# Performance work log

Measured on AMD Instinct MI355X. Metric: run time of the kernel, lower is better.

Reference implementation:

```python
import jax, jax.numpy as jnp
import numpy as np

B, N, D = 128, 64, 768
H, DK = 32, 24
L, TE, TD, VP = 4, 32, 40, 512


def setup_inputs():
    key = jax.random.key(0)
    ks = jax.random.split(key, 20)
    s = 0.02
    return {
        "node_reps": jax.random.normal(ks[0], (B, N, D), jnp.float32),
        "distance": jax.random.randint(ks[1], (B, N, N), 0, TD, jnp.int32),
        "connection_reps": jax.random.randint(ks[2], (B, N, N), 0, TE, jnp.int32),
        "shortest_path_feature_trajectory": jax.random.randint(ks[3], (B, N, N, L, 3), 0, VP, jnp.int32),
        "mask": jnp.zeros((B, N), jnp.bool_),
        "W_qkv": jax.random.normal(ks[4], (D, 3 * H * DK), jnp.float32) * s,
        "b_qkv": jnp.zeros((3 * H * DK,), jnp.float32),
        "W_out": jax.random.normal(ks[5], (H * DK, D), jnp.float32) * s,
        "b_out": jnp.zeros((D,), jnp.float32),
        "edge_q_table": jax.random.normal(ks[6], (TE, H, DK), jnp.float32) * s,
        "edge_k_table": jax.random.normal(ks[7], (TE, H, DK), jnp.float32) * s,
        "dist_q_table": jax.random.normal(ks[8], (TD, H, DK), jnp.float32) * s,
        "dist_k_table": jax.random.normal(ks[9], (TD, H, DK), jnp.float32) * s,
        "path_emb": jax.random.normal(ks[10], (VP, H), jnp.float32) * s,
        "path_pos_w": jax.random.normal(ks[11], (L, H), jnp.float32) * s,
        "edge_val_table": jax.random.normal(ks[12], (TE, H, DK), jnp.float32) * s,
        "dist_val_table": jax.random.normal(ks[13], (TD, H, DK), jnp.float32) * s,
        "toeplitz_r": jnp.ones((H, N), jnp.float32) + jax.random.normal(ks[14], (H, N), jnp.float32) * s,
        "toeplitz_c": jnp.ones((H, N), jnp.float32) + jax.random.normal(ks[15], (H, N), jnp.float32) * s,
    }


def _relpos_bias(q, k, types, Eq, Ek):
    # bias[b,h,i,j] = q[b,h,i] . Ek[t(i,j),h] + k[b,h,j] . Eq[t(i,j),h]
    Bx, Hx, Nx, _ = q.shape
    qb = jnp.einsum('bhid,thd->bhit', q, Ek)   # per-type query bias [B,H,N,T]
    kb = jnp.einsum('bhjd,thd->bhtj', k, Eq)   # per-type key bias   [B,H,T,N]
    idx = jnp.broadcast_to(types[:, None], (Bx, Hx, Nx, Nx))
    return jnp.take_along_axis(qb, idx, axis=3) + jnp.take_along_axis(kb, idx, axis=2)


def _path_bias(traj, dist, path_emb, path_pos_w):
    # Graphormer-style shortest-path bias: per-position embedded (3-way) edge
    # features dotted with per-position head weights, normalized by path length.
    bias = 0.0
    for l in range(traj.shape[3]):          # small fixed loop over path positions
        for f in range(3):                  # 3 discrete edge features per hop
            bias = bias + path_emb[traj[:, :, :, l, f]] * path_pos_w[l]  # [B,N,N,H]
    denom = jnp.clip(dist.astype(jnp.float32), 1.0, None)
    return (bias / denom[..., None]).transpose(0, 3, 1, 2)  # [B,H,N,N]


def _comp_values(a, types, Vt):
    # z[b,h,i,d] = sum_j a[b,h,i,j] * Vt[type(i,j),h,d]  (post-softmax value add)
    onehot = jax.nn.one_hot(types, Vt.shape[0], dtype=a.dtype)  # [B,N,N,T]
    s = jnp.einsum('bhij,bijt->bhit', a, onehot)
    return jnp.einsum('bhit,thd->bhid', s, Vt)


def reference(node_reps, distance, connection_reps, shortest_path_feature_trajectory, mask,
              W_qkv, b_qkv, W_out, b_out, edge_q_table, edge_k_table,
              dist_q_table, dist_k_table, path_emb, path_pos_w,
              edge_val_table, dist_val_table, toeplitz_r, toeplitz_c):
    Bx, Nx, Dx = node_reps.shape
    qkv = (node_reps @ W_qkv + b_qkv).reshape(Bx, Nx, 3, H, DK)
    q = qkv[:, :, 0].transpose(0, 2, 1, 3)  # [B,H,N,dk]
    k = qkv[:, :, 1].transpose(0, 2, 1, 3)
    v = qkv[:, :, 2].transpose(0, 2, 1, 3)
    a = jnp.einsum('bhid,bhjd->bhij', q, k)
    a = a + _relpos_bias(q, k, connection_reps, edge_q_table, edge_k_table)
    a = a + _relpos_bias(q, k, distance, dist_q_table, dist_k_table)
    a = a + _path_bias(shortest_path_feature_trajectory, distance, path_emb, path_pos_w)
    a = a * (DK ** -0.5)  # scale applied after bias addition, as in the original
    a = jnp.where(mask[:, None, None, :], -jnp.inf, a)
    a = jax.nn.softmax(a, axis=3)
    # post-softmax per-head Toeplitz modulation: T[h,i,j] = r[h,j-i] (j>=i) else c[h,i-j]
    off = jnp.arange(Nx)[None, :] - jnp.arange(Nx)[:, None]
    toep = jnp.where(off >= 0, toeplitz_r[:, jnp.clip(off, 0)], toeplitz_c[:, jnp.clip(-off, 0)])
    a = a * toep[None]  # attention dropout is identity at eval
    z = jnp.einsum('bhij,bhjd->bhid', a, v)
    z = z + _comp_values(a, connection_reps, edge_val_table)
    z = z + _comp_values(a, distance, dist_val_table)
    z = z.transpose(0, 2, 1, 3).reshape(Bx, Nx, H * DK)
    return z @ W_out + b_out
```

## Files before the change

kernel.cpp:

```cpp
#include <hip/hip_runtime.h>
#include <hip/hip_fp16.h>

#define Bb 128
#define Nn 64
#define Dd 768
#define Hh 32
#define DKk 24
#define Ll 4
#define TEe 32
#define TDd 40

typedef __attribute__((ext_vector_type(8))) short short8_t;
typedef __attribute__((ext_vector_type(8))) _Float16 half8_t;
typedef __attribute__((ext_vector_type(4))) float f32x4;

__device__ __forceinline__ void gload16(const void* g, void* l) {
    __builtin_amdgcn_global_load_lds((const __attribute__((address_space(1))) void*)g,
                                     (__attribute__((address_space(3))) void*)l, 16, 0, 0);
}

__global__ __launch_bounds__(256) void split_f16_kernel(
    const float4* __restrict__ src, __half* __restrict__ hi,
    __half* __restrict__ lo, int n4)
{
    int i = blockIdx.x * 256 + threadIdx.x;
    if (i >= n4) return;
    float4 v = src[i];
    float vv[4] = {v.x, v.y, v.z, v.w};
    unsigned short hbits[4], lbits[4];
#pragma unroll
    for (int e = 0; e < 4; e++) {
        __half h = __float2half(vv[e]);
        __half l = __float2half(vv[e] - __half2float(h));
        hbits[e] = __half_as_ushort(h);
        lbits[e] = __half_as_ushort(l);
    }
    uint2 ph, pl;
    ph.x = (unsigned)hbits[0] | ((unsigned)hbits[1] << 16);
    ph.y = (unsigned)hbits[2] | ((unsigned)hbits[3] << 16);
    pl.x = (unsigned)lbits[0] | ((unsigned)lbits[1] << 16);
    pl.y = (unsigned)lbits[2] | ((unsigned)lbits[3] << 16);
    *(uint2*)&hi[i * 4] = ph;
    *(uint2*)&lo[i * 4] = pl;
}

#define MFMA16(a, b, c) __builtin_amdgcn_mfma_f32_16x16x32_f16((a), (b), (c), 0, 0, 0)

template <typename OutT>
__global__ __launch_bounds__(256, 3) void gemm_f16x2_kernel(
    const __half* __restrict__ Ah, const __half* __restrict__ Al,
    const __half* __restrict__ Bh,
    const float* __restrict__ bias, OutT* __restrict__ C,
    int M, int N, int K)
{
    __shared__ char smem[49152] __attribute__((aligned(16)));

    const int t = threadIdx.x;
    const int lane = t & 63, w = t >> 6;
    const int wr = w >> 1, wc = w & 1;

    const int nbx = gridDim.x;
    int id = blockIdx.y * nbx + blockIdx.x;
    const int nwg = nbx * gridDim.y;
    if ((nwg & 7) == 0) {
        id = (id & 7) * (nwg >> 3) + (id >> 3);
    }
    const int rowBase = (id / nbx) * 128, colBase = (id % nbx) * 128;

    const int m0 = t >> 2;
    const int g0 = (t & 3) ^ ((m0 >> 1) & 3);
    const size_t aoff0 = (size_t)(rowBase + m0) * K + g0 * 8;
    const size_t aoff1 = aoff0 + (size_t)64 * K;
    const size_t boff0 = (size_t)(colBase + m0) * K + g0 * 8;
    const size_t boff1 = boff0 + (size_t)64 * K;
    const int lb = w * 1024;

    int offA[4], offB[4];
    const int lr = lane & 15, koff = lane >> 4;
#pragma unroll
    for (int i = 0; i < 4; i++) {
        int ma = wr * 64 + i * 16 + lr;
        offA[i] = ma * 32 + ((koff ^ ((ma >> 1) & 3)) << 3);
        int nb = wc * 64 + i * 16 + lr;
        offB[i] = nb * 32 + ((koff ^ ((nb >> 1) & 3)) << 3);
    }

    f32x4 acc[4][4];
#pragma unroll
    for (int i = 0; i < 4; i++)
#pragma unroll
        for (int j = 0; j < 4; j++) acc[i][j] = (f32x4){0.f, 0.f, 0.f, 0.f};

    auto stage = [&](int buf, int k0) {
        char* base = smem + buf * 24576;
        gload16(Ah + aoff0 + k0, base + lb);
        gload16(Ah + aoff1 + k0, base + lb + 4096);
        gload16(Al + aoff0 + k0, base + 8192 + lb);
        gload16(Al + aoff1 + k0, base + 8192 + lb + 4096);
        gload16(Bh + boff0 + k0, base + 16384 + lb);
        gload16(Bh + boff1 + k0, base + 16384 + lb + 4096);
    };

    stage(0, 0);
    __syncthreads();

    const int T = K / 32;
    for (int it = 0; it < T; it++) {
        const int cur = it & 1;
        if (it + 1 < T) stage(cur ^ 1, (it + 1) * 32);

        const short* sAh = (const short*)(smem + cur * 24576);
        const short* sAl = (const short*)(smem + cur * 24576 + 8192);
        const short* sBh = (const short*)(smem + cur * 24576 + 16384);

        half8_t ah[4], al[4], bh[4];
#pragma unroll
        for (int i = 0; i < 4; i++) {
            ah[i] = *(const half8_t*)(sAh + offA[i]);
            al[i] = *(const half8_t*)(sAl + offA[i]);
            bh[i] = *(const half8_t*)(sBh + offB[i]);
        }
#pragma unroll
        for (int i = 0; i < 4; i++)
#pragma unroll
            for (int j = 0; j < 4; j++) {
                acc[i][j] = MFMA16(al[i], bh[j], acc[i][j]);
                acc[i][j] = MFMA16(ah[i], bh[j], acc[i][j]);
            }
        __syncthreads();
    }

    const int crow = rowBase + wr * 64 + (lane >> 4) * 4;
    const int ccol = colBase + wc * 64 + (lane & 15);
#pragma unroll
    for (int j = 0; j < 4; j++) {
        int col = ccol + j * 16;
        float bv = bias[col];
#pragma unroll
        for (int i = 0; i < 4; i++) {
#pragma unroll
            for (int r = 0; r < 4; r++) {
                float x = acc[i][j][r] + bv;
                if constexpr (__is_same(OutT, __half))
                    C[(size_t)(crow + i * 16 + r) * N + col] = __float2half(x);
                else
                    C[(size_t)(crow + i * 16 + r) * N + col] = x;
            }
        }
    }
}

__device__ __forceinline__ void do_transpose(
    const float* __restrict__ W, __half* __restrict__ th,
    int K, int N, int k0, int n0, char* uls, int t)
{
    float (*tile)[33] = (float(*)[33])uls;
    const int c = t & 31, r0 = t >> 5;
    for (int rr = r0; rr < 32; rr += 8)
        tile[rr][c] = W[(size_t)(k0 + rr) * N + n0 + c];
    __syncthreads();
    for (int rr = r0; rr < 32; rr += 8)
        th[(size_t)(n0 + rr) * K + k0 + c] = __float2half(tile[c][rr]);
}

__global__ __launch_bounds__(256, 2) void prep_kernel(
    const float* __restrict__ Wqkv, __half* __restrict__ wqth,
    const float* __restrict__ Wout, __half* __restrict__ woth,
    const int* __restrict__ traj, const int* __restrict__ dist,
    const int* __restrict__ conn,
    const float* __restrict__ path_emb, const float* __restrict__ path_pos_w,
    __half* __restrict__ pbias, unsigned short* __restrict__ packed)
{
    __shared__ char uls[69632] __attribute__((aligned(16)));
    const int id = blockIdx.x;
    const int t = threadIdx.x;

    if (id < 1728) {
        do_transpose(Wqkv, wqth, 768, 2304, (id % 24) * 32, (id / 24) * 32, uls, t);
        return;
    }
    if (id < 2304) {
        int id2 = id - 1728;
        do_transpose(Wout, woth, 768, 768, (id2 % 24) * 32, (id2 / 24) * 32, uls, t);
        return;
    }

    __half* sPE  = (__half*)uls;
    __half* sOut = (__half*)(uls + 32768);
    const int q = id - 2304;
    const int b = q >> 3, pt = q & 7;
    const int ch = t & 7;
    const int pl = t >> 3;

    const long pair0 = (long)b * 4096 + pt * 512;

    for (int e = t; e < 512; e += 256) {
        long gp = pair0 + e;
        packed[gp] = (unsigned short)((unsigned)conn[gp] | ((unsigned)dist[gp] << 8));
    }

    for (int e = t; e < 4096; e += 256) {
        float4 v = ((const float4*)path_emb)[e];
        __half2 h0 = __floats2half2_rn(v.x, v.y);
        __half2 h1 = __floats2half2_rn(v.z, v.w);
        uint2 pk;
        pk.x = *(unsigned*)&h0;
        pk.y = *(unsigned*)&h1;
        *(uint2*)&sPE[e * 4] = pk;
    }
    __half2 pwa[4], pwb[4];
#pragma unroll
    for (int l = 0; l < 4; l++) {
        float4 wv = *(const float4*)&path_pos_w[l * 32 + ch * 4];
        pwa[l] = __floats2half2_rn(wv.x, wv.y);
        pwb[l] = __floats2half2_rn(wv.z, wv.w);
    }
    __syncthreads();

    for (int rnd = 0; rnd < 16; rnd++) {
        int p = rnd * 32 + pl;
        long gp = pair0 + p;
        const int4* tp = (const int4*)(traj + gp * 12);
        int4 t0 = tp[0], t1 = tp[1], t2 = tp[2];
        int idxs[12] = {t0.x, t0.y, t0.z, t0.w, t1.x, t1.y, t1.z, t1.w,
                        t2.x, t2.y, t2.z, t2.w};
        __half2 acc0 = __float2half2_rn(0.f);
        __half2 acc1 = __float2half2_rn(0.f);
#pragma unroll
        for (int l = 0; l < 4; l++) {
            uint2 r0 = *(const uint2*)&sPE[idxs[l * 3 + 0] * 32 + ch * 4];
            uint2 r1 = *(const uint2*)&sPE[idxs[l * 3 + 1] * 32 + ch * 4];
            uint2 r2 = *(const uint2*)&sPE[idxs[l * 3 + 2] * 32 + ch * 4];
            __half2 s0 = __hadd2(__hadd2(*(__half2*)&r0.x, *(__half2*)&r1.x), *(__half2*)&r2.x);
            __half2 s1 = __hadd2(__hadd2(*(__half2*)&r0.y, *(__half2*)&r1.y), *(__half2*)&r2.y);
            acc0 = __hfma2(s0, pwa[l], acc0);
            acc1 = __hfma2(s1, pwb[l], acc1);
        }
        int dd = dist[gp];
        __half2 hi2 = __float2half2_rn(1.0f / (float)(dd > 1 ? dd : 1));
        acc0 = __hmul2(acc0, hi2);
        acc1 = __hmul2(acc1, hi2);
        uint2 pk;
        pk.x = *(unsigned*)&acc0;
        pk.y = *(unsigned*)&acc1;
        *(uint2*)&sOut[p * 36 + ch * 4] = pk;
    }
    __syncthreads();

    __half* outBase = pbias + (size_t)b * 32 * 4096 + pt * 512;
    for (int e = t; e < 32 * 512; e += 256) {
        int hh = e >> 9, p = e & 511;
        outBase[(size_t)hh * 4096 + p] = sOut[p * 36 + hh];
    }
}

#define IDX32(row, k) ((row)*32 + (((((k) >> 3) ^ (((row) >> 1) & 3))) << 3) + ((k) & 7))
#define IDX64(row, k) ((row)*64 + (((((k) >> 3) ^ ((row) & 7))) << 3) + ((k) & 7))
#define LDH32(base, row, k) (*(const half8_t*)(sm + (base) + IDX32(row, k) * 2))
#define LDH64(base, row, k) (*(const half8_t*)(sm + (base) + IDX64(row, k) * 2))

__global__ __launch_bounds__(256, 5) void attn_kernel(
    const __half* __restrict__ qkv,
    const unsigned short* __restrict__ packed,
    const __half* __restrict__ pbias,
    const float* __restrict__ eq, const float* __restrict__ ek,
    const float* __restrict__ dq, const float* __restrict__ dk,
    const float* __restrict__ ev, const float* __restrict__ dv,
    const float* __restrict__ tr, const float* __restrict__ tcp,
    __half* __restrict__ zh, __half* __restrict__ zl)
{
    __shared__ char sm[30336] __attribute__((aligned(16)));
    const int h = blockIdx.x, b = blockIdx.y;
    const int t = threadIdx.x;
    const int lane = t & 63, w = t >> 6;
    const int c = lane & 15, kg = lane >> 4;

    enum { TEK = 0, TEQ = 2048, TDK = 4096, TDQ = 7168,
           GQBE = 10240, GKBE = 14592, GQBD = 18944, GKBD = 24384,
           TOEP = 29824,
           PH = 0, VTH = 8192, VET = 12288, VDT = 14336,
           BINE = 17920, BIND = 23040 };

    const size_t qkvRow = (size_t)(b * 64) * 2304 + h * 24;
    const unsigned short* tpk = packed + (size_t)b * 4096;
    const int ibase = 16 * w + kg * 4;

    half8_t zf8 = (half8_t)(_Float16)0.f;
    half8_t aQ = zf8, aK = zf8, bK0 = zf8, bK1 = zf8, bK2 = zf8, bK3 = zf8;
    if (kg < 3) {
        const __half* qp = qkv + qkvRow + kg * 8;
        aQ  = *(const half8_t*)(qp + (size_t)(16 * w + c) * 2304);
        aK  = *(const half8_t*)(qp + (size_t)(16 * w + c) * 2304 + 768);
        bK0 = *(const half8_t*)(qp + (size_t)(c) * 2304 + 768);
        bK1 = *(const half8_t*)(qp + (size_t)(16 + c) * 2304 + 768);
        bK2 = *(const half8_t*)(qp + (size_t)(32 + c) * 2304 + 768);
        bK3 = *(const half8_t*)(qp + (size_t)(48 + c) * 2304 + 768);
    }
    unsigned short tvv[16];
    __half pbvh[16];
    {
        const __half* pbb = pbias + ((size_t)(b * 32 + h)) * 4096;
#pragma unroll
        for (int j4 = 0; j4 < 4; j4++) {
            int jj = 16 * j4 + c;
#pragma unroll
            for (int r = 0; r < 4; r++) {
                int i = ibase + r;
                tvv[j4 * 4 + r] = tpk[i * 64 + jj];
                pbvh[j4 * 4 + r] = pbb[i * 64 + jj];
            }
        }
    }
    short8_t v8 = (short8_t)(short)0;
    const int vi = t / 3, voc = t - vi * 3;
    if (t < 192)
        v8 = *(const short8_t*)(qkv + qkvRow + (size_t)vi * 2304 + 1536 + voc * 8);

    for (int f = t; f < 864; f += 256) {
        int row = f / 6, d0 = (f - row * 6) * 4;
        const float* src; int base, lrow;
        if (row < 32)       { src = ek + ((size_t)row * 32 + h) * 24 + d0; base = TEK; lrow = row; }
        else if (row < 64)  { src = eq + ((size_t)(row - 32) * 32 + h) * 24 + d0; base = TEQ; lrow = row - 32; }
        else if (row < 104) { src = dk + ((size_t)(row - 64) * 32 + h) * 24 + d0; base = TDK; lrow = row - 64; }
        else                { src = dq + ((size_t)(row - 104) * 32 + h) * 24 + d0; base = TDQ; lrow = row - 104; }
        float4 v = *(const float4*)src;
        __half2 p0 = __floats2half2_rn(v.x, v.y);
        __half2 p1 = __floats2half2_rn(v.z, v.w);
        uint2 pk; pk.x = *(unsigned*)&p0; pk.y = *(unsigned*)&p1;
        *(uint2*)(sm + base + IDX32(lrow, d0) * 2) = pk;
    }
    if (t < 208) {
        int base, row, oct;
        if (t < 32)       { base = TEK; row = t; oct = 3; }
        else if (t < 64)  { base = TEQ; row = t - 32; oct = 3; }
        else if (t < 136) { int u = t - 64;
                            if (u < 40) { base = TDK; row = u; oct = 3; }
                            else { int v2 = u - 40; base = TDK; row = 40 + (v2 >> 2); oct = v2 & 3; } }
        else              { int u = t - 136;
                            if (u < 40) { base = TDQ; row = u; oct = 3; }
                            else { int v2 = u - 40; base = TDQ; row = 40 + (v2 >> 2); oct = v2 & 3; } }
        uint4 z4; z4.x = z4.y = z4.z = z4.w = 0u;
        *(uint4*)(sm + base + IDX32(row, oct * 8) * 2) = z4;
    }
    if (t < 64) ((float*)(sm + TOEP))[63 + t] = tr[h * 64 + t];
    else if (t < 127) { int d2 = t - 63; ((float*)(sm + TOEP))[63 - d2] = tcp[h * 64 + d2]; }
    __syncthreads();

    f32x4 accS[4];
    {
        accS[0] = MFMA16(aQ, bK0, ((f32x4){0.f, 0.f, 0.f, 0.f}));
        accS[1] = MFMA16(aQ, bK1, ((f32x4){0.f, 0.f, 0.f, 0.f}));
        accS[2] = MFMA16(aQ, bK2, ((f32x4){0.f, 0.f, 0.f, 0.f}));
        accS[3] = MFMA16(aQ, bK3, ((f32x4){0.f, 0.f, 0.f, 0.f}));
        const int i0 = ibase;
#pragma unroll
        for (int tab = 0; tab < 4; tab++) {
            half8_t aF = (tab == 1 || tab == 3) ? aK : aQ;
            int tabBase = (tab == 0) ? TEK : (tab == 1) ? TEQ : (tab == 2) ? TDK : TDQ;
            int gtBase  = (tab == 0) ? GQBE : (tab == 1) ? GKBE : (tab == 2) ? GQBD : GKBD;
            int ntiles  = (tab < 2) ? 2 : 3;
            int nrows   = (tab < 2) ? 32 : 40;
            for (int t4 = 0; t4 < ntiles; t4++) {
                half8_t bF = LDH32(tabBase, 16 * t4 + c, kg * 8);
                f32x4 a = MFMA16(aF, bF, ((f32x4){0.f, 0.f, 0.f, 0.f}));
                int tcol = 16 * t4 + c;
                if (tcol < nrows) {
                    __half2 p0 = __floats2half2_rn(a[0], a[1]);
                    __half2 p1 = __floats2half2_rn(a[2], a[3]);
                    uint2 pk; pk.x = *(unsigned*)&p0; pk.y = *(unsigned*)&p1;
                    *(uint2*)(sm + gtBase + (tcol * 68 + i0) * 2) = pk;
                }
            }
        }
    }
    __syncthreads();

    {
        float p[4][4];
#pragma unroll
        for (int j4 = 0; j4 < 4; j4++) {
            int jj = 16 * j4 + c;
#pragma unroll
            for (int r = 0; r < 4; r++) {
                int i = ibase + r;
                int ce = (int)(tvv[j4 * 4 + r] & 255u), cd = (int)(tvv[j4 * 4 + r] >> 8);
                float se = __half2float(*(const __half*)(sm + GQBE + (ce * 68 + i) * 2))
                         + __half2float(*(const __half*)(sm + GKBE + (ce * 68 + jj) * 2));
                float sd = __half2float(*(const __half*)(sm + GQBD + (cd * 68 + i) * 2))
                         + __half2float(*(const __half*)(sm + GKBD + (cd * 68 + jj) * 2));
                float s = (accS[j4][r] + __half2float(pbvh[j4 * 4 + r])) + (se + sd);
                p[j4][r] = s * 0.2944888931f;
            }
        }
        float inv[4];
#pragma unroll
        for (int r = 0; r < 4; r++) {
            float m = fmaxf(fmaxf(p[0][r], p[1][r]), fmaxf(p[2][r], p[3][r]));
            m = fmaxf(m, __shfl_xor(m, 1));
            m = fmaxf(m, __shfl_xor(m, 2));
            m = fmaxf(m, __shfl_xor(m, 4));
            m = fmaxf(m, __shfl_xor(m, 8));
            float s = 0.f;
#pragma unroll
            for (int j4 = 0; j4 < 4; j4++) { p[j4][r] = exp2f(p[j4][r] - m); s += p[j4][r]; }
            s += __shfl_xor(s, 1);
            s += __shfl_xor(s, 2);
            s += __shfl_xor(s, 4);
            s += __shfl_xor(s, 8);
            inv[r] = 1.0f / s;
        }
        const float* tp = (const float*)(sm + TOEP);
#pragma unroll
        for (int j4 = 0; j4 < 4; j4++) {
#pragma unroll
            for (int r = 0; r < 4; r++) {
                int i = ibase + r, j = 16 * j4 + c;
                float tpv = tp[63 + j - i];
                float val = p[j4][r] * inv[r] * tpv;
                *(unsigned short*)(sm + PH + IDX64(i, j) * 2) =
                    __half_as_ushort(__float2half(val));
            }
        }
    }
    __syncthreads();

    for (int e = t; e < 2752; e += 256) {
        uint2 z2; z2.x = z2.y = 0u;
        *(uint2*)(sm + 8192 + e * 8) = z2;
    }
    __syncthreads();

    if (t < 192) {
#pragma unroll
        for (int e2 = 0; e2 < 8; e2++) {
            *(short*)(sm + VTH + IDX64(voc * 8 + e2, vi) * 2) = v8[e2];
        }
    }
    for (int f = t; f < 432; f += 256) {
        int tcol = f / 6, d0 = (f - tcol * 6) * 4;
        const float* src = (tcol < 32) ? ev + ((size_t)tcol * 32 + h) * 24 + d0
                                       : dv + ((size_t)(tcol - 32) * 32 + h) * 24 + d0;
        float4 v = *(const float4*)src;
        float vv[4] = {v.x, v.y, v.z, v.w};
#pragma unroll
        for (int r2 = 0; r2 < 4; r2++) {
            int d = d0 + r2;
            if (tcol < 32)
                *(unsigned short*)(sm + VET + IDX32(d, tcol) * 2) =
                    __half_as_ushort(__float2half(vv[r2]));
            else
                *(unsigned short*)(sm + VDT + (d * 56 + (tcol - 32)) * 2) =
                    __half_as_ushort(__float2half(vv[r2]));
        }
    }
    __syncthreads();

    {
        for (int rnd = 0; rnd < 2; rnd++) {
            if ((w >> 1) == rnd) {
                int kind = w & 1;
                int i = lane;
                const unsigned short* ip = tpk + i * 64 + rnd * 32;
                __half* bins = (__half*)(sm + (kind ? BIND : BINE));
                int stride = kind ? 56 : 40;
#pragma unroll
                for (int blk = 0; blk < 4; blk++) {
                    int o = rnd * 4 + blk;
                    short8_t ph8 = *(const short8_t*)(sm + PH + (i * 64 + ((o ^ (i & 7)) << 3)) * 2);
                    uint4 pw = *(const uint4*)(ip + blk * 8);
                    unsigned dw[4] = {pw.x, pw.y, pw.z, pw.w};
#pragma unroll
                    for (int e2 = 0; e2 < 8; e2++) {
                        unsigned ent = (dw[e2 >> 1] >> ((e2 & 1) * 16)) & 0xFFFFu;
                        int ty = kind ? (int)(ent >> 8) : (int)(ent & 255u);
                        __half pv = __ushort_as_half((unsigned short)ph8[e2]);
                        __half* ap = bins + i * stride + ty;
                        *ap = __hadd(*ap, pv);
                    }
                }
            }
            __syncthreads();
        }
    }

    {
        half8_t aP0 = LDH64(PH, 16 * w + c, kg * 8);
        half8_t aP1 = LDH64(PH, 16 * w + c, 32 + kg * 8);
        half8_t aBE = *(const half8_t*)(sm + BINE + ((16 * w + c) * 40 + kg * 8) * 2);
        half8_t aD0 = *(const half8_t*)(sm + BIND + ((16 * w + c) * 56 + kg * 8) * 2);
        half8_t zf = (half8_t)(_Float16)0.f;
        half8_t aD1 = (kg < 2)
            ? *(const half8_t*)(sm + BIND + ((16 * w + c) * 56 + 32 + kg * 8) * 2) : zf;
#pragma unroll
        for (int d4 = 0; d4 < 2; d4++) {
            int drow = 16 * d4 + c;
            f32x4 a = (f32x4){0.f, 0.f, 0.f, 0.f};
            a = MFMA16(aP0, LDH64(VTH, drow, kg * 8), a);
            a = MFMA16(aP1, LDH64(VTH, drow, 32 + kg * 8), a);
            a = MFMA16(aBE, LDH32(VET, drow, kg * 8), a);
            a = MFMA16(aD0, *(const half8_t*)(sm + VDT + (drow * 56 + kg * 8) * 2), a);
            half8_t bD1 = (kg < 2)
                ? *(const half8_t*)(sm + VDT + (drow * 56 + 32 + kg * 8) * 2) : zf;
            a = MFMA16(aD1, bD1, a);
            int d = d4 * 16 + c;
            if (d < 24) {
#pragma unroll
                for (int r = 0; r < 4; r++) {
                    int i = 16 * w + kg * 4 + r;
                    size_t zi = ((size_t)(b * 64 + i)) * 768 + h * 24 + d;
                    float x = a[r];
                    __half hx = __float2half(x);
                    zh[zi] = hx;
                    zl[zi] = __float2half(x - __half2float(hx));
                }
            }
        }
    }
}

extern "C" void kernel_launch(void* const* d_in, const int* in_sizes, int n_in,
                              void* d_out, int out_size, void* d_ws, size_t ws_size,
                              hipStream_t stream) {
    const float* node = (const float*)d_in[0];
    const int* dist   = (const int*)d_in[1];
    const int* conn   = (const int*)d_in[2];
    const int* traj   = (const int*)d_in[3];
    const float* Wqkv = (const float*)d_in[5];
    const float* bqkv = (const float*)d_in[6];
    const float* Wout = (const float*)d_in[7];
    const float* bout = (const float*)d_in[8];
    const float* eqT  = (const float*)d_in[9];
    const float* ekT  = (const float*)d_in[10];
    const float* dqT  = (const float*)d_in[11];
    const float* dkT  = (const float*)d_in[12];
    const float* pemb = (const float*)d_in[13];
    const float* ppw  = (const float*)d_in[14];
    const float* evT  = (const float*)d_in[15];
    const float* dvT  = (const float*)d_in[16];
    const float* trp  = (const float*)d_in[17];
    const float* tcp  = (const float*)d_in[18];
    float* out = (float*)d_out;

    char* ws = (char*)d_ws;
    __half* qkvh = (__half*)ws;
    __half* pb   = (__half*)(ws + 37748736);
    __half* wqth = (__half*)(ws + 71303168);
    __half* woth = (__half*)(ws + 74842112);
    unsigned short* pkd = (unsigned short*)(ws + 76021760);
    __half* nodeh = (__half*)(ws + 109051904);
    __half* nodel = nodeh + 8192 * 768;
    __half* zhp = nodeh;
    __half* zlp = nodel;

    split_f16_kernel<<<6144, 256, 0, stream>>>((const float4*)node, nodeh, nodel,
                                               8192 * 768 / 4);

    prep_kernel<<<3328, 256, 0, stream>>>(Wqkv, wqth, Wout, woth,
                                          traj, dist, conn, pemb, ppw, pb, pkd);

    gemm_f16x2_kernel<__half><<<dim3(18, 64), 256, 0, stream>>>(
        nodeh, nodel, wqth, bqkv, qkvh, 8192, 2304, 768);

    attn_kernel<<<dim3(Hh, Bb), 256, 0, stream>>>(
        qkvh, pkd, pb, eqT, ekT, dqT, dkT, evT, dvT, trp, tcp, zhp, zlp);

    gemm_f16x2_kernel<float><<<dim3(6, 64), 256, 0, stream>>>(
        zhp, zlp, woth, bout, out, 8192, 768, 768);
}
```

Baseline: 327.2 us.

## Fuse node split into prep kernel, shrink its LDS, add MFMA priority hints

```diff
diff --git a/kernel.cpp b/kernel.cpp
--- a/kernel.cpp
+++ b/kernel.cpp
@@ -17,31 +17,6 @@
 __device__ __forceinline__ void gload16(const void* g, void* l) {
     __builtin_amdgcn_global_load_lds((const __attribute__((address_space(1))) void*)g,
                                      (__attribute__((address_space(3))) void*)l, 16, 0, 0);
-}
-
-__global__ __launch_bounds__(256) void split_f16_kernel(
-    const float4* __restrict__ src, __half* __restrict__ hi,
-    __half* __restrict__ lo, int n4)
-{
-    int i = blockIdx.x * 256 + threadIdx.x;
-    if (i >= n4) return;
-    float4 v = src[i];
-    float vv[4] = {v.x, v.y, v.z, v.w};
-    unsigned short hbits[4], lbits[4];
-#pragma unroll
-    for (int e = 0; e < 4; e++) {
-        __half h = __float2half(vv[e]);
-        __half l = __float2half(vv[e] - __half2float(h));
-        hbits[e] = __half_as_ushort(h);
-        lbits[e] = __half_as_ushort(l);
-    }
-    uint2 ph, pl;
-    ph.x = (unsigned)hbits[0] | ((unsigned)hbits[1] << 16);
-    ph.y = (unsigned)hbits[2] | ((unsigned)hbits[3] << 16);
-    pl.x = (unsigned)lbits[0] | ((unsigned)lbits[1] << 16);
-    pl.y = (unsigned)lbits[2] | ((unsigned)lbits[3] << 16);
-    *(uint2*)&hi[i * 4] = ph;
-    *(uint2*)&lo[i * 4] = pl;
 }
 
 #define MFMA16(a, b, c) __builtin_amdgcn_mfma_f32_16x16x32_f16((a), (b), (c), 0, 0, 0)
@@ -163,7 +138,9 @@
         th[(size_t)(n0 + rr) * K + k0 + c] = __float2half(tile[c][rr]);
 }
 
-__global__ __launch_bounds__(256, 2) void prep_kernel(
+__global__ __launch_bounds__(256, 3) void prep_kernel(
+    const float4* __restrict__ node, __half* __restrict__ nodeh,
+    __half* __restrict__ nodel,
     const float* __restrict__ Wqkv, __half* __restrict__ wqth,
     const float* __restrict__ Wout, __half* __restrict__ woth,
     const int* __restrict__ traj, const int* __restrict__ dist,
@@ -171,24 +148,46 @@
     const float* __restrict__ path_emb, const float* __restrict__ path_pos_w,
     __half* __restrict__ pbias, unsigned short* __restrict__ packed)
 {
-    __shared__ char uls[69632] __attribute__((aligned(16)));
+    __shared__ char uls[51200] __attribute__((aligned(16)));
     const int id = blockIdx.x;
     const int t = threadIdx.x;
 
-    if (id < 1728) {
-        do_transpose(Wqkv, wqth, 768, 2304, (id % 24) * 32, (id / 24) * 32, uls, t);
+    if (id >= 3328) {
+        int i = (id - 3328) * 256 + t;
+        if (i >= 8192 * 768 / 4) return;
+        float4 v = node[i];
+        float vv[4] = {v.x, v.y, v.z, v.w};
+        unsigned short hbits[4], lbits[4];
+#pragma unroll
+        for (int e = 0; e < 4; e++) {
+            __half h = __float2half(vv[e]);
+            __half l = __float2half(vv[e] - __half2float(h));
+            hbits[e] = __half_as_ushort(h);
+            lbits[e] = __half_as_ushort(l);
+        }
+        uint2 ph, pl2;
+        ph.x = (unsigned)hbits[0] | ((unsigned)hbits[1] << 16);
+        ph.y = (unsigned)hbits[2] | ((unsigned)hbits[3] << 16);
+        pl2.x = (unsigned)lbits[0] | ((unsigned)lbits[1] << 16);
+        pl2.y = (unsigned)lbits[2] | ((unsigned)lbits[3] << 16);
+        *(uint2*)&nodeh[i * 4] = ph;
+        *(uint2*)&nodel[i * 4] = pl2;
         return;
     }
-    if (id < 2304) {
-        int id2 = id - 1728;
+    if (id >= 2752) {
+        int id2 = id - 2752;
         do_transpose(Wout, woth, 768, 768, (id2 % 24) * 32, (id2 / 24) * 32, uls, t);
         return;
     }
+    if (id >= 1024) {
+        int id2 = id - 1024;
+        do_transpose(Wqkv, wqth, 768, 2304, (id2 % 24) * 32, (id2 / 24) * 32, uls, t);
+        return;
+    }
 
     __half* sPE  = (__half*)uls;
     __half* sOut = (__half*)(uls + 32768);
-    const int q = id - 2304;
-    const int b = q >> 3, pt = q & 7;
+    const int b = id >> 3, pt = id & 7;
     const int ch = t & 7;
     const int pl = t >> 3;
 
@@ -217,40 +216,42 @@
     }
     __syncthreads();
 
-    for (int rnd = 0; rnd < 16; rnd++) {
-        int p = rnd * 32 + pl;
-        long gp = pair0 + p;
-        const int4* tp = (const int4*)(traj + gp * 12);
-        int4 t0 = tp[0], t1 = tp[1], t2 = tp[2];
-        int idxs[12] = {t0.x, t0.y, t0.z, t0.w, t1.x, t1.y, t1.z, t1.w,
-                        t2.x, t2.y, t2.z, t2.w};
-        __half2 acc0 = __float2half2_rn(0.f);
-        __half2 acc1 = __float2half2_rn(0.f);
-#pragma unroll
-        for (int l = 0; l < 4; l++) {
-            uint2 r0 = *(const uint2*)&sPE[idxs[l * 3 + 0] * 32 + ch * 4];
-            uint2 r1 = *(const uint2*)&sPE[idxs[l * 3 + 1] * 32 + ch * 4];
-            uint2 r2 = *(const uint2*)&sPE[idxs[l * 3 + 2] * 32 + ch * 4];
-            __half2 s0 = __hadd2(__hadd2(*(__half2*)&r0.x, *(__half2*)&r1.x), *(__half2*)&r2.x);
-            __half2 s1 = __hadd2(__hadd2(*(__half2*)&r0.y, *(__half2*)&r1.y), *(__half2*)&r2.y);
-            acc0 = __hfma2(s0, pwa[l], acc0);
-            acc1 = __hfma2(s1, pwb[l], acc1);
-        }
-        int dd = dist[gp];
-        __half2 hi2 = __float2half2_rn(1.0f / (float)(dd > 1 ? dd : 1));
-        acc0 = __hmul2(acc0, hi2);
-        acc1 = __hmul2(acc1, hi2);
-        uint2 pk;
-        pk.x = *(unsigned*)&acc0;
-        pk.y = *(unsigned*)&acc1;
-        *(uint2*)&sOut[p * 36 + ch * 4] = pk;
-    }
-    __syncthreads();
-
-    __half* outBase = pbias + (size_t)b * 32 * 4096 + pt * 512;
-    for (int e = t; e < 32 * 512; e += 256) {
-        int hh = e >> 9, p = e & 511;
-        outBase[(size_t)hh * 4096 + p] = sOut[p * 36 + hh];
+    for (int cchunk = 0; cchunk < 2; cchunk++) {
+        for (int rr = 0; rr < 8; rr++) {
+            int p_local = rr * 32 + pl;
+            long gp = pair0 + cchunk * 256 + p_local;
+            const int4* tp = (const int4*)(traj + gp * 12);
+            int4 t0 = tp[0], t1 = tp[1], t2 = tp[2];
+            int idxs[12] = {t0.x, t0.y, t0.z, t0.w, t1.x, t1.y, t1.z, t1.w,
+                            t2.x, t2.y, t2.z, t2.w};
+            __half2 acc0 = __float2half2_rn(0.f);
+            __half2 acc1 = __float2half2_rn(0.f);
+#pragma unroll
+            for (int l = 0; l < 4; l++) {
+                uint2 r0 = *(const uint2*)&sPE[idxs[l * 3 + 0] * 32 + ch * 4];
+                uint2 r1 = *(const uint2*)&sPE[idxs[l * 3 + 1] * 32 + ch * 4];
+                uint2 r2 = *(const uint2*)&sPE[idxs[l * 3 + 2] * 32 + ch * 4];
+                __half2 s0 = __hadd2(__hadd2(*(__half2*)&r0.x, *(__half2*)&r1.x), *(__half2*)&r2.x);
+                __half2 s1 = __hadd2(__hadd2(*(__half2*)&r0.y, *(__half2*)&r1.y), *(__half2*)&r2.y);
+                acc0 = __hfma2(s0, pwa[l], acc0);
+                acc1 = __hfma2(s1, pwb[l], acc1);
+            }
+            int dd = dist[gp];
+            __half2 hi2 = __float2half2_rn(1.0f / (float)(dd > 1 ? dd : 1));
+            acc0 = __hmul2(acc0, hi2);
+            acc1 = __hmul2(acc1, hi2);
+            uint2 pk;
+            pk.x = *(unsigned*)&acc0;
+            pk.y = *(unsigned*)&acc1;
+            *(uint2*)&sOut[p_local * 36 + ch * 4] = pk;
+        }
+        __syncthreads();
+        __half* outBase = pbias + (size_t)b * 32 * 4096 + pt * 512 + cchunk * 256;
+        for (int e = t; e < 8192; e += 256) {
+            int hh = e >> 8, p2 = e & 255;
+            outBase[(size_t)hh * 4096 + p2] = sOut[p2 * 36 + hh];
+        }
+        __syncthreads();
     }
 }
 
@@ -348,6 +349,7 @@
 
     f32x4 accS[4];
     {
+        __builtin_amdgcn_s_setprio(1);
         accS[0] = MFMA16(aQ, bK0, ((f32x4){0.f, 0.f, 0.f, 0.f}));
         accS[1] = MFMA16(aQ, bK1, ((f32x4){0.f, 0.f, 0.f, 0.f}));
         accS[2] = MFMA16(aQ, bK2, ((f32x4){0.f, 0.f, 0.f, 0.f}));
@@ -372,6 +374,7 @@
                 }
             }
         }
+        __builtin_amdgcn_s_setprio(0);
     }
     __syncthreads();
 
@@ -424,12 +427,6 @@
     }
     __syncthreads();
 
-    for (int e = t; e < 2752; e += 256) {
-        uint2 z2; z2.x = z2.y = 0u;
-        *(uint2*)(sm + 8192 + e * 8) = z2;
-    }
-    __syncthreads();
-
     if (t < 192) {
 #pragma unroll
         for (int e2 = 0; e2 < 8; e2++) {
@@ -453,6 +450,10 @@
                     __half_as_ushort(__float2half(vv[r2]));
         }
     }
+    for (int e = t; e < 768; e += 256) {
+        uint4 z4; z4.x = z4.y = z4.z = z4.w = 0u;
+        *(uint4*)(sm + 17920 + e * 16) = z4;
+    }
     __syncthreads();
 
     {
@@ -484,6 +485,7 @@
     }
 
     {
+        __builtin_amdgcn_s_setprio(1);
         half8_t aP0 = LDH64(PH, 16 * w + c, kg * 8);
         half8_t aP1 = LDH64(PH, 16 * w + c, 32 + kg * 8);
         half8_t aBE = *(const half8_t*)(sm + BINE + ((16 * w + c) * 40 + kg * 8) * 2);
@@ -491,6 +493,7 @@
         half8_t zf = (half8_t)(_Float16)0.f;
         half8_t aD1 = (kg < 2)
             ? *(const half8_t*)(sm + BIND + ((16 * w + c) * 56 + 32 + kg * 8) * 2) : zf;
+        f32x4 av[2];
 #pragma unroll
         for (int d4 = 0; d4 < 2; d4++) {
             int drow = 16 * d4 + c;
@@ -502,13 +505,18 @@
             half8_t bD1 = (kg < 2)
                 ? *(const half8_t*)(sm + VDT + (drow * 56 + 32 + kg * 8) * 2) : zf;
             a = MFMA16(aD1, bD1, a);
+            av[d4] = a;
+        }
+        __builtin_amdgcn_s_setprio(0);
+#pragma unroll
+        for (int d4 = 0; d4 < 2; d4++) {
             int d = d4 * 16 + c;
             if (d < 24) {
 #pragma unroll
                 for (int r = 0; r < 4; r++) {
                     int i = 16 * w + kg * 4 + r;
                     size_t zi = ((size_t)(b * 64 + i)) * 768 + h * 24 + d;
-                    float x = a[r];
+                    float x = av[d4][r];
                     __half hx = __float2half(x);
                     zh[zi] = hx;
                     zl[zi] = __float2half(x - __half2float(hx));
@@ -552,10 +560,8 @@
     __half* zhp = nodeh;
     __half* zlp = nodel;
 
-    split_f16_kernel<<<6144, 256, 0, stream>>>((const float4*)node, nodeh, nodel,
-                                               8192 * 768 / 4);
-
-    prep_kernel<<<3328, 256, 0, stream>>>(Wqkv, wqth, Wout, woth,
+    prep_kernel<<<9472, 256, 0, stream>>>((const float4*)node, nodeh, nodel,
+                                          Wqkv, wqth, Wout, woth,
                                           traj, dist, conn, pemb, ppw, pb, pkd);
 
     gemm_f16x2_kernel<__half><<<dim3(18, 64), 256, 0, stream>>>(
```

Measured after the change: 313.1 us. 4.3% less time.
